# Optimization experiments

Hardware: AMD Instinct MI355X
Metric: run time of the kernel (lower is better)

## Reference

```python
import jax, jax.numpy as jnp
import numpy as np

H = 16  # heads
DH = 64  # dim_head
SCALE = DH ** -0.5


def rotate_half(x):
    x1, x2 = jnp.split(x, 2, axis=-1)
    return jnp.concatenate([-x2, x1], axis=-1)


def apply_rope(pos, t):
    # pos: [n, d] broadcast over [b, h, n, d]
    return t * jnp.cos(pos) + rotate_half(t) * jnp.sin(pos)


def setup_inputs() -> dict:
    key = jax.random.key(0)
    ks = jax.random.split(key, 6)
    B, N, D = 4, 2048, 1024
    inner = H * DH
    x = jax.random.normal(ks[0], (B, N, D), dtype=jnp.float32)
    rotary_emb = jax.random.normal(ks[1], (N, DH), dtype=jnp.float32)
    Wq = jax.random.normal(ks[2], (D, inner), dtype=jnp.float32) / np.sqrt(D)
    Wkv = jax.random.normal(ks[3], (D, 2 * inner), dtype=jnp.float32) / np.sqrt(D)
    Wout = jax.random.normal(ks[4], (inner, D), dtype=jnp.float32) / np.sqrt(inner)
    bout = jnp.zeros((D,), dtype=jnp.float32)
    return {"x": x, "rotary_emb": rotary_emb, "Wq": Wq, "Wkv": Wkv, "Wout": Wout, "bout": bout}


def reference(x, rotary_emb, Wq, Wkv, Wout, bout):
    B, N, D = x.shape
    # QKV projections (self-attention: context = x)
    q = x @ Wq                       # [b, n, h*d]
    kv = x @ Wkv                     # [b, n, 2*h*d]
    k, v = jnp.split(kv, 2, axis=-1)

    def to_heads(t):
        return t.reshape(B, N, H, DH).transpose(0, 2, 1, 3)  # [b, h, n, d]

    q, k, v = to_heads(q), to_heads(k), to_heads(v)
    q = apply_rope(rotary_emb, q)
    k = apply_rope(rotary_emb, k)

    # scaled dot-product attention
    scores = jnp.einsum('bhid,bhjd->bhij', q, k) * SCALE
    attn = jax.nn.softmax(scores, axis=-1)
    out = jnp.einsum('bhij,bhjd->bhid', attn, v)  # [b, h, n, d]
    out = out.transpose(0, 2, 1, 3).reshape(B, N, H * DH)
    return out @ Wout + bout
```

## Files before the change

### kernel.cpp

```cpp
#include <hip/hip_runtime.h>

#define BB 4
#define NN 2048
#define DD 1024
#define HH 16
#define DHH 64
#define MM (BB*NN)
#define QS 3072

typedef unsigned short u16;
typedef __attribute__((ext_vector_type(8))) short short8;
typedef __attribute__((ext_vector_type(4))) float floatx4;

#if __has_builtin(__builtin_amdgcn_exp2f)
#define EXP2F __builtin_amdgcn_exp2f
#else
#define EXP2F exp2f
#endif

__device__ __forceinline__ u16 f2bf(float f) {
  union { float f; unsigned u; } v; v.f = f;
  unsigned u = v.u;
  return (u16)((u + 0x7fffu + ((u >> 16) & 1u)) >> 16);
}
__device__ __forceinline__ float bf2f(u16 h) {
  union { unsigned u; float f; } v; v.u = ((unsigned)h) << 16;
  return v.f;
}
__device__ __forceinline__ unsigned fbits(float f) {
  union { float f; unsigned u; } v; v.f = f; return v.u;
}
__device__ __forceinline__ unsigned pkbf(float lo, float hi) {
#if __has_builtin(__builtin_amdgcn_perm)
  return __builtin_amdgcn_perm(fbits(hi), fbits(lo), 0x07060302u);
#else
  return (fbits(lo) >> 16) | (fbits(hi) & 0xffff0000u);
#endif
}
__device__ __forceinline__ void gll16(const u16* g, u16* l) {
  __builtin_amdgcn_global_load_lds((const __attribute__((address_space(1))) unsigned int*)g,
                                   (__attribute__((address_space(3))) unsigned int*)l, 16, 0, 0);
}
__device__ __forceinline__ int toff(int row, int kc) {
  int pr = row >> 1;
  int c = (((row & 1) << 2) + kc) ^ (pr & 7);
  return pr * 64 + c * 8;
}

#define SOFTMAX_SCALE 0.18033688f
#define SOFTMAX_BIAS  -28.8539008f

__global__ __launch_bounds__(256) void cvt_kernel(const float* __restrict__ in,
                                                  u16* __restrict__ out, int n) {
  int i = (blockIdx.x * 256 + threadIdx.x) * 4;
  if (i >= n) return;
  float4 v = *(const float4*)(in + i);
  u16 o[4] = {f2bf(v.x), f2bf(v.y), f2bf(v.z), f2bf(v.w)};
  *(uint2*)(out + i) = *(uint2*)o;
}

__global__ __launch_bounds__(256) void tcvt3_kernel(const float* __restrict__ Wq,
                                                    const float* __restrict__ Wkv,
                                                    const float* __restrict__ Wout,
                                                    u16* __restrict__ WT,
                                                    u16* __restrict__ WoutT) {
  __shared__ float t[64][65];
  int bx = blockIdx.x;
  const float* src;
  u16* dst;
  int C, c0;
  if (bx < 16)      { src = Wq;   dst = WT;                       C = 1024; c0 = bx * 64; }
  else if (bx < 48) { src = Wkv;  dst = WT + (size_t)DD * DD;     C = 2048; c0 = (bx - 16) * 64; }
  else              { src = Wout; dst = WoutT;                    C = 1024; c0 = (bx - 48) * 64; }
  const int R = 1024;
  int r0 = blockIdx.y * 64;
  int tid = threadIdx.x;
#pragma unroll
  for (int i = 0; i < 16; ++i) {
    int lin = i * 256 + tid;
    int rr = lin >> 6, cc = lin & 63;
    t[rr][cc] = src[(size_t)(r0 + rr) * C + c0 + cc];
  }
  __syncthreads();
#pragma unroll
  for (int i = 0; i < 16; ++i) {
    int lin = i * 256 + tid;
    int rr = lin >> 6, cc = lin & 63;
    dst[(size_t)(c0 + rr) * R + r0 + cc] = f2bf(t[cc][rr]);
  }
}

__global__ __launch_bounds__(256) void rope_tab_kernel(const float* __restrict__ rot,
                                                       float2* __restrict__ tab) {
  int i = blockIdx.x * 256 + threadIdx.x;
  float p = rot[i];
  float s, c;
  __sincosf(p, &s, &c);
  tab[i] = make_float2(c, s);
}

__global__ __launch_bounds__(512, 2) void gemm_qk(const u16* __restrict__ A,
                                                  const u16* __restrict__ Bt,
                                                  u16* __restrict__ qd,
                                                  u16* __restrict__ kd,
                                                  const float2* __restrict__ tab) {
  const int K = DD;
  const int NT = K / 64;
  __shared__ __align__(16) u16 lds[65536];
  int tid = threadIdx.x;
  int wave = tid >> 6, lane = tid & 63;
  int q4 = lane >> 4, l16 = lane & 15;
  int wr = wave >> 2, wc = wave & 3;

  int flat = blockIdx.y * 8 + blockIdx.x;
  int wg = (flat & 7) * 32 + (flat >> 3);
  int bx = wg & 7, by = wg >> 3;
  int m0 = by * 256, n0 = bx * 256;

  const u16* Ag = A + (size_t)m0 * K;
  const u16* Bg = Bt + (size_t)n0 * K;

  int spr = tid >> 3, sct = tid & 7, su = sct ^ (spr & 7);
  int srow = spr * 2 + (su >> 2);
  int skc = (su & 3) * 8;
  size_t so = (size_t)srow * K + skc;

  int toffA[8], toffB[4];
#pragma unroll
  for (int mi = 0; mi < 8; ++mi) toffA[mi] = wr * 4096 + toff(mi * 16 + l16, q4);
#pragma unroll
  for (int ni = 0; ni < 4; ++ni)
    toffB[ni] = (wc >> 1) * 4096 + toff((wc & 1) * 64 + ni * 16 + l16, q4);

  floatx4 acc[8][4];
#pragma unroll
  for (int mi = 0; mi < 8; ++mi)
#pragma unroll
    for (int ni = 0; ni < 4; ++ni) acc[mi][ni] = (floatx4){0.f, 0.f, 0.f, 0.f};

  auto stageHalf = [&](int t, int mat, int kh) {
    const u16* src = (mat ? Bg : Ag) + so + t * 64 + kh * 32;
    u16* dst = lds + (t & 1) * 32768 + mat * 16384 + kh * 8192 + wave * 512;
    gll16(src, dst);
    gll16(src + (size_t)128 * K, dst + 4096);
  };

  stageHalf(0, 1, 0); stageHalf(0, 0, 0); stageHalf(0, 1, 1); stageHalf(0, 0, 1);
  stageHalf(1, 1, 0); stageHalf(1, 0, 0); stageHalf(1, 1, 1);
  __builtin_amdgcn_s_waitcnt(0x0F76);
  __builtin_amdgcn_s_barrier();

#pragma unroll
  for (int t = 0; t < NT; ++t) {
    const u16* Ab = lds + (t & 1) * 32768;
    const u16* Bb = Ab + 16384;
    short8 af[4], bfq[4];

#pragma unroll
    for (int ni = 0; ni < 4; ++ni) bfq[ni] = *(const short8*)(Bb + toffB[ni]);
#pragma unroll
    for (int f = 0; f < 4; ++f) af[f] = *(const short8*)(Ab + toffA[f]);
    if (t + 1 < NT) stageHalf(t + 1, 0, 1);
    __builtin_amdgcn_s_barrier();
    __builtin_amdgcn_s_waitcnt(0xC07F);
    __builtin_amdgcn_s_setprio(1);
#pragma unroll
    for (int f = 0; f < 4; ++f)
#pragma unroll
      for (int ni = 0; ni < 4; ++ni)
        acc[f][ni] = __builtin_amdgcn_mfma_f32_16x16x32_bf16(bfq[ni], af[f], acc[f][ni], 0, 0, 0);
    __builtin_amdgcn_s_setprio(0);
    __builtin_amdgcn_s_barrier();

#pragma unroll
    for (int f = 0; f < 4; ++f) af[f] = *(const short8*)(Ab + toffA[4 + f]);
    if (t + 2 < NT) stageHalf(t + 2, 1, 0);
    __builtin_amdgcn_s_barrier();
    __builtin_amdgcn_s_waitcnt(0xC07F);
    __builtin_amdgcn_s_setprio(1);
#pragma unroll
    for (int f = 0; f < 4; ++f)
#pragma unroll
      for (int ni = 0; ni < 4; ++ni)
        acc[4 + f][ni] = __builtin_amdgcn_mfma_f32_16x16x32_bf16(bfq[ni], af[f], acc[4 + f][ni], 0, 0, 0);
    __builtin_amdgcn_s_setprio(0);
    __builtin_amdgcn_s_barrier();

#pragma unroll
    for (int ni = 0; ni < 4; ++ni) bfq[ni] = *(const short8*)(Bb + 8192 + toffB[ni]);
#pragma unroll
    for (int f = 0; f < 4; ++f) af[f] = *(const short8*)(Ab + 8192 + toffA[f]);
    if (t + 2 < NT) stageHalf(t + 2, 0, 0);
    __builtin_amdgcn_s_barrier();
    __builtin_amdgcn_s_waitcnt(0xC07F);
    __builtin_amdgcn_s_setprio(1);
#pragma unroll
    for (int f = 0; f < 4; ++f)
#pragma unroll
      for (int ni = 0; ni < 4; ++ni)
        acc[f][ni] = __builtin_amdgcn_mfma_f32_16x16x32_bf16(bfq[ni], af[f], acc[f][ni], 0, 0, 0);
    __builtin_amdgcn_s_setprio(0);
    __builtin_amdgcn_s_barrier();

#pragma unroll
    for (int f = 0; f < 4; ++f) af[f] = *(const short8*)(Ab + 8192 + toffA[4 + f]);
    if (t + 2 < NT) stageHalf(t + 2, 1, 1);
    __builtin_amdgcn_s_barrier();
    __builtin_amdgcn_s_waitcnt(0xC07F);
    __builtin_amdgcn_s_setprio(1);
#pragma unroll
    for (int f = 0; f < 4; ++f)
#pragma unroll
      for (int ni = 0; ni < 4; ++ni)
        acc[4 + f][ni] = __builtin_amdgcn_mfma_f32_16x16x32_bf16(bfq[ni], af[f], acc[4 + f][ni], 0, 0, 0);
    __builtin_amdgcn_s_setprio(0);
    if (t == NT - 2) __builtin_amdgcn_s_waitcnt(0x0F70);
    else if (t < NT - 2) __builtin_amdgcn_s_waitcnt(0x0F76);
    __builtin_amdgcn_s_barrier();
  }

  int h = (n0 + wc * 64) >> 6;
  u16* dst = (h < 16) ? qd : kd;
  int hh = h & 15;
  float scl = (h < 16) ? SOFTMAX_SCALE : 1.0f;
  int b = m0 >> 11;
  int tokbase = (m0 & (NN - 1)) + wr * 128;
#pragma unroll
  for (int mi = 0; mi < 8; ++mi) {
    int tok = tokbase + mi * 16 + l16;
    u16* rowp = dst + ((size_t)(b * HH + hh) * NN + tok) * 64;
    const float2* tb = tab + tok * 64;
#pragma unroll
    for (int ni = 0; ni < 2; ++ni) {
      int d0 = ni * 16 + q4 * 4;
      u16 plo[4], phi[4];
#pragma unroll
      for (int r = 0; r < 4; ++r) {
        float2 cs0 = tb[d0 + r];
        float2 cs1 = tb[d0 + r + 32];
        float v0 = acc[mi][ni][r], v1 = acc[mi][ni + 2][r];
        plo[r] = f2bf((v0 * cs0.x - v1 * cs0.y) * scl);
        phi[r] = f2bf((v1 * cs1.x + v0 * cs1.y) * scl);
      }
      *(uint2*)(rowp + d0) = *(uint2*)plo;
      *(uint2*)(rowp + d0 + 32) = *(uint2*)phi;
    }
  }
}

__global__ __launch_bounds__(256) void gemm_v(const u16* __restrict__ A,
                                              const u16* __restrict__ Bt,
                                              u16* __restrict__ vt) {
  const int K = DD;
  __shared__ __align__(16) u16 lds[16384];
  int tid = threadIdx.x;
  int wave = tid >> 6, lane = tid & 63;
  int q4 = lane >> 4, l16 = lane & 15;

  int flat = blockIdx.y * 8 + blockIdx.x;
  int wg = (flat & 7) * 64 + (flat >> 3);
  int bx = wg & 7, by = wg >> 3;
  int m0 = by * 128, n0 = bx * 128;

  int wm = (wave >> 1) * 64, wn = (wave & 1) * 64;

  const u16* Ag = A + (size_t)m0 * K;
  const u16* Bg = Bt + (size_t)(2048 + n0) * K;
  int o1 = tid, o2 = tid + 256;
  int pr1 = o1 >> 3, c1 = (o1 & 7) ^ (pr1 & 7);
  int row1 = pr1 * 2 + (c1 >> 2), kc1 = (c1 & 3) * 8;
  int pr2 = o2 >> 3, c2 = (o2 & 7) ^ (pr2 & 7);
  int row2 = pr2 * 2 + (c2 >> 2), kc2 = (c2 & 3) * 8;
  int d1 = wave * 512, d2 = 2048 + wave * 512;

  int foA[4], foB[4];
#pragma unroll
  for (int i = 0; i < 4; ++i) {
    foA[i] = toff(wm + i * 16 + l16, q4);
    foB[i] = toff(wn + i * 16 + l16, q4);
  }

  floatx4 acc[4][4];
#pragma unroll
  for (int mi = 0; mi < 4; ++mi)
#pragma unroll
    for (int ni = 0; ni < 4; ++ni) acc[mi][ni] = (floatx4){0.f, 0.f, 0.f, 0.f};

  gll16(Ag + (size_t)row1 * K + kc1, lds + d1);
  gll16(Ag + (size_t)row2 * K + kc2, lds + d2);
  gll16(Bg + (size_t)row1 * K + kc1, lds + 8192 + d1);
  gll16(Bg + (size_t)row2 * K + kc2, lds + 8192 + d2);

  for (int k0 = 0, it = 0; k0 < K; k0 += 32, ++it) {
    int boff = (it & 1) * 4096;
    if (k0 + 32 < K) {
      int nboff = 4096 - boff;
      int kn = k0 + 32;
      gll16(Ag + (size_t)row1 * K + kn + kc1, lds + nboff + d1);
      gll16(Ag + (size_t)row2 * K + kn + kc2, lds + nboff + d2);
      gll16(Bg + (size_t)row1 * K + kn + kc1, lds + 8192 + nboff + d1);
      gll16(Bg + (size_t)row2 * K + kn + kc2, lds + 8192 + nboff + d2);
      __builtin_amdgcn_s_waitcnt(0x0F74);
    } else {
      __builtin_amdgcn_s_waitcnt(0x0F70);
    }
    __builtin_amdgcn_s_barrier();
    const u16* Ac = lds + boff;
    const u16* Bc = lds + 8192 + boff;
    short8 af[4], bfr[4];
#pragma unroll
    for (int i = 0; i < 4; ++i) {
      af[i]  = *(const short8*)(Ac + foA[i]);
      bfr[i] = *(const short8*)(Bc + foB[i]);
    }
#pragma unroll
    for (int mi = 0; mi < 4; ++mi)
#pragma unroll
      for (int ni = 0; ni < 4; ++ni)
        acc[mi][ni] = __builtin_amdgcn_mfma_f32_16x16x32_bf16(af[mi], bfr[ni], acc[mi][ni], 0, 0, 0);
    __builtin_amdgcn_s_barrier();
  }

  int h = (n0 + wn) >> 6;
#pragma unroll
  for (int mi = 0; mi < 4; ++mi) {
    int mbase = m0 + wm + mi * 16 + q4 * 4;
    int b = mbase >> 11;
    int nn = mbase & (NN - 1);
    u16* base = vt + (size_t)(b * HH + h) * (NN * 64) + (nn >> 6) * 4096 + (nn & 63);
#pragma unroll
    for (int ni = 0; ni < 4; ++ni) {
      int d = ni * 16 + l16;
      u16 p[4] = {f2bf(acc[mi][ni][0]), f2bf(acc[mi][ni][1]),
                  f2bf(acc[mi][ni][2]), f2bf(acc[mi][ni][3])};
      *(uint2*)(base + d * 64) = *(uint2*)p;
    }
  }
}

__global__ __launch_bounds__(256) void gemm_out(const u16* __restrict__ A,
                                                const u16* __restrict__ Bt,
                                                float* __restrict__ Cout,
                                                const float* __restrict__ bias,
                                                int M, int N, int K) {
  __shared__ __align__(16) u16 lds[16384];
  int tid = threadIdx.x;
  int wave = tid >> 6, lane = tid & 63;
  int q4 = lane >> 4, l16 = lane & 15;
  int m0 = blockIdx.y * 128, n0 = blockIdx.x * 128;
  int wm = (wave >> 1) * 64, wn = (wave & 1) * 64;

  const u16* Ag = A + (size_t)m0 * K;
  const u16* Bg = Bt + (size_t)n0 * K;
  int o1 = tid, o2 = tid + 256;
  int pr1 = o1 >> 3, c1 = (o1 & 7) ^ (pr1 & 7);
  int row1 = pr1 * 2 + (c1 >> 2), kc1 = (c1 & 3) * 8;
  int pr2 = o2 >> 3, c2 = (o2 & 7) ^ (pr2 & 7);
  int row2 = pr2 * 2 + (c2 >> 2), kc2 = (c2 & 3) * 8;
  int d1 = wave * 512, d2 = 2048 + wave * 512;

  int foA[4], foB[4];
#pragma unroll
  for (int i = 0; i < 4; ++i) {
    foA[i] = toff(wm + i * 16 + l16, q4);
    foB[i] = toff(wn + i * 16 + l16, q4);
  }

  floatx4 acc[4][4];
#pragma unroll
  for (int mi = 0; mi < 4; ++mi)
#pragma unroll
    for (int ni = 0; ni < 4; ++ni) acc[mi][ni] = (floatx4){0.f, 0.f, 0.f, 0.f};

  gll16(Ag + (size_t)row1 * K + kc1, lds + d1);
  gll16(Ag + (size_t)row2 * K + kc2, lds + d2);
  gll16(Bg + (size_t)row1 * K + kc1, lds + 8192 + d1);
  gll16(Bg + (size_t)row2 * K + kc2, lds + 8192 + d2);

  for (int k0 = 0, it = 0; k0 < K; k0 += 32, ++it) {
    int boff = (it & 1) * 4096;
    if (k0 + 32 < K) {
      int nboff = 4096 - boff;
      int kn = k0 + 32;
      gll16(Ag + (size_t)row1 * K + kn + kc1, lds + nboff + d1);
      gll16(Ag + (size_t)row2 * K + kn + kc2, lds + nboff + d2);
      gll16(Bg + (size_t)row1 * K + kn + kc1, lds + 8192 + nboff + d1);
      gll16(Bg + (size_t)row2 * K + kn + kc2, lds + 8192 + nboff + d2);
      __builtin_amdgcn_s_waitcnt(0x0F74);
    } else {
      __builtin_amdgcn_s_waitcnt(0x0F70);
    }
    __builtin_amdgcn_s_barrier();
    const u16* Ac = lds + boff;
    const u16* Bc = lds + 8192 + boff;
    short8 af[4], bfr[4];
#pragma unroll
    for (int i = 0; i < 4; ++i) {
      af[i]  = *(const short8*)(Ac + foA[i]);
      bfr[i] = *(const short8*)(Bc + foB[i]);
    }
#pragma unroll
    for (int mi = 0; mi < 4; ++mi)
#pragma unroll
      for (int ni = 0; ni < 4; ++ni)
        acc[mi][ni] = __builtin_amdgcn_mfma_f32_16x16x32_bf16(af[mi], bfr[ni], acc[mi][ni], 0, 0, 0);
    __builtin_amdgcn_s_barrier();
  }

#pragma unroll
  for (int ni = 0; ni < 4; ++ni) {
    int col = n0 + wn + ni * 16 + l16;
    float bval = bias[col];
#pragma unroll
    for (int mi = 0; mi < 4; ++mi) {
#pragma unroll
      for (int r = 0; r < 4; ++r) {
        int row = m0 + wm + mi * 16 + q4 * 4 + r;
        Cout[(size_t)row * N + col] = acc[mi][ni][r] + bval;
      }
    }
  }
}

__global__ __launch_bounds__(512, 4) void attn_kernel(const u16* __restrict__ qd,
                                                      const u16* __restrict__ kd,
                                                      const u16* __restrict__ vt,
                                                      u16* __restrict__ ao) {
  __shared__ __align__(16) u16 lds[16384];

  int tid = threadIdx.x, wave = tid >> 6, lane = tid & 63;
  int q4 = lane >> 4, l16 = lane & 15;
  int qt = blockIdx.x, bh = blockIdx.y, b = bh >> 4, h = bh & 15;
  const u16* qbh = qd + (size_t)bh * NN * 64;
  const u16* kbh = kd + (size_t)bh * NN * 64;
  const u16* vbh = vt + (size_t)bh * NN * 64;

  int srow = wave * 8 + (lane >> 3);
  int g = ((lane & 7) ^ ((lane >> 3) & 7)) * 8;
  int prow = ((srow >> 2) & 3) * 8 + ((srow >> 4) & 1) * 4 + (srow & 3) + ((srow >> 5) & 1) * 32;

#pragma unroll
  for (int it = 0; it < 4; ++it)
    gll16(qbh + (size_t)(qt * 256 + it * 64 + srow) * 64 + g, lds + (it * 64 + wave * 8) * 64);
  __builtin_amdgcn_s_waitcnt(0x0F70);
  __builtin_amdgcn_s_barrier();

  short8 aq[2][2];
#pragma unroll
  for (int mi = 0; mi < 2; ++mi)
#pragma unroll
    for (int ks = 0; ks < 2; ++ks) {
      int row = wave * 32 + mi * 16 + l16;
      aq[mi][ks] = *(const short8*)(lds + row * 64 + (((ks * 4 + q4) ^ (row & 7)) * 8));
    }
  __builtin_amdgcn_s_waitcnt(0xC07F);
  __builtin_amdgcn_s_barrier();

  gll16(kbh + (size_t)prow * 64 + g, lds + wave * 512);
  gll16(vbh + (size_t)srow * 64 + g, lds + 8192 + wave * 512);

  union { unsigned u[4]; short8 s8; } ones;
#pragma unroll
  for (int i = 0; i < 4; ++i) ones.u[i] = 0x3F803F80u;

  floatx4 lacc[2];
  floatx4 o[2][4];
#pragma unroll
  for (int mi = 0; mi < 2; ++mi) {
    lacc[mi] = (floatx4){0.f, 0.f, 0.f, 0.f};
#pragma unroll
    for (int di = 0; di < 4; ++di) o[mi][di] = (floatx4){0.f, 0.f, 0.f, 0.f};
  }

  for (int j0 = 0, itn = 0; j0 < NN; j0 += 64, ++itn) {
    int coff = (itn & 1) * 4096;
    if (j0 + 64 < NN) {
      int noff = 4096 - coff;
      gll16(kbh + (size_t)(j0 + 64 + prow) * 64 + g, lds + noff + wave * 512);
      gll16(vbh + (size_t)((j0 >> 6) + 1) * 4096 + srow * 64 + g, lds + 8192 + noff + wave * 512);
      __builtin_amdgcn_s_waitcnt(0x0F72);
    } else {
      __builtin_amdgcn_s_waitcnt(0x0F70);
    }
    __builtin_amdgcn_s_barrier();

    const u16* Kc = lds + coff;
    const u16* Vc = lds + 8192 + coff;

    floatx4 s[4][2];
#pragma unroll
    for (int kg = 0; kg < 4; ++kg)
#pragma unroll
      for (int mi = 0; mi < 2; ++mi)
        s[kg][mi] = (floatx4){SOFTMAX_BIAS, SOFTMAX_BIAS, SOFTMAX_BIAS, SOFTMAX_BIAS};
#pragma unroll
    for (int ks = 0; ks < 2; ++ks) {
      short8 kf[4];
#pragma unroll
      for (int kg = 0; kg < 4; ++kg) {
        int row = kg * 16 + l16;
        kf[kg] = *(const short8*)(Kc + row * 64 + (((ks * 4 + q4) ^ (row & 7)) * 8));
      }
#pragma unroll
      for (int kg = 0; kg < 4; ++kg)
#pragma unroll
        for (int mi = 0; mi < 2; ++mi)
          s[kg][mi] = __builtin_amdgcn_mfma_f32_16x16x32_bf16(kf[kg], aq[mi][ks], s[kg][mi], 0, 0, 0);
    }

    unsigned pk[4][2][2];
#pragma unroll
    for (int kg = 0; kg < 4; ++kg)
#pragma unroll
      for (int mi = 0; mi < 2; ++mi) {
        float e0 = EXP2F(s[kg][mi][0]);
        float e1 = EXP2F(s[kg][mi][1]);
        float e2 = EXP2F(s[kg][mi][2]);
        float e3 = EXP2F(s[kg][mi][3]);
        pk[kg][mi][0] = pkbf(e0, e1);
        pk[kg][mi][1] = pkbf(e2, e3);
      }

#pragma unroll
    for (int ks = 0; ks < 2; ++ks) {
      short8 vf[4];
#pragma unroll
      for (int di = 0; di < 4; ++di) {
        int row = di * 16 + l16;
        vf[di] = *(const short8*)(Vc + row * 64 + (((ks * 4 + q4) ^ (row & 7)) * 8));
      }
#pragma unroll
      for (int mi = 0; mi < 2; ++mi) {
        union { unsigned u[4]; short8 s8; } bw;
        bw.u[0] = pk[2 * ks][mi][0];
        bw.u[1] = pk[2 * ks][mi][1];
        bw.u[2] = pk[2 * ks + 1][mi][0];
        bw.u[3] = pk[2 * ks + 1][mi][1];
        lacc[mi] = __builtin_amdgcn_mfma_f32_16x16x32_bf16(ones.s8, bw.s8, lacc[mi], 0, 0, 0);
#pragma unroll
        for (int di = 0; di < 4; ++di)
          o[mi][di] = __builtin_amdgcn_mfma_f32_16x16x32_bf16(vf[di], bw.s8, o[mi][di], 0, 0, 0);
      }
    }
    __builtin_amdgcn_s_barrier();
  }

  float rinv[2];
#pragma unroll
  for (int mi = 0; mi < 2; ++mi) rinv[mi] = 1.0f / lacc[mi][0];

#pragma unroll
  for (int mi = 0; mi < 2; ++mi) {
    int qrow = qt * 256 + wave * 32 + mi * 16 + l16;
    size_t base = (size_t)(b * NN + qrow) * DD + h * DHH + q4 * 4;
#pragma unroll
    for (int di = 0; di < 4; ++di)
#pragma unroll
      for (int r = 0; r < 4; ++r)
        ao[base + di * 16 + r] = f2bf(o[mi][di][r] * rinv[mi]);
  }
}

extern "C" void kernel_launch(void* const* d_in, const int* in_sizes, int n_in,
                              void* d_out, int out_size, void* d_ws, size_t ws_size,
                              hipStream_t stream) {
  const float* x    = (const float*)d_in[0];
  const float* rot  = (const float*)d_in[1];
  const float* Wq   = (const float*)d_in[2];
  const float* Wkv  = (const float*)d_in[3];
  const float* Wout = (const float*)d_in[4];
  const float* bout = (const float*)d_in[5];
  float* out = (float*)d_out;

  char* ws = (char*)d_ws;
  size_t off = 0;
  auto alloc = [&](size_t bytes) {
    void* p = ws + off;
    off = (off + bytes + 255) & ~(size_t)255;
    return p;
  };
  u16*    xb    = (u16*)alloc((size_t)MM * DD * 2);
  u16*    WT    = (u16*)alloc((size_t)QS * DD * 2);
  u16*    WoutT = (u16*)alloc((size_t)DD * DD * 2);
  float2* tab   = (float2*)alloc((size_t)NN * DHH * 8);
  u16*    qdb   = (u16*)alloc((size_t)MM * DD * 2);
  u16*    kdb   = (u16*)alloc((size_t)MM * DD * 2);
  u16*    vtt   = (u16*)alloc((size_t)MM * DD * 2);
  u16*    ao    = (u16*)alloc((size_t)MM * DD * 2);

  cvt_kernel<<<(MM * DD / 4) / 256, 256, 0, stream>>>(x, xb, MM * DD);
  tcvt3_kernel<<<dim3(64, 16), 256, 0, stream>>>(Wq, Wkv, Wout, WT, WoutT);
  rope_tab_kernel<<<(NN * DHH) / 256, 256, 0, stream>>>(rot, tab);

  gemm_qk<<<dim3(8, 32), 512, 0, stream>>>(xb, WT, qdb, kdb, tab);
  gemm_v<<<dim3(8, 64), 256, 0, stream>>>(xb, WT, vtt);

  attn_kernel<<<dim3(NN / 256, BB * HH), 512, 0, stream>>>(qdb, kdb, vtt, ao);

  gemm_out<<<dim3(DD / 128, MM / 128), 256, 0, stream>>>(ao, WoutT, out, bout, MM, DD, DD);
}
```

Baseline: 270.6 us.

## Software-pipeline attention loop with 4-stage KV ring and XCD-aware block remap

Restructures the attention main loop so that the QK^T MFMAs for tile t are issued alongside the exp and PV MFMAs for tile t-1, using two score register sets. KV staging grows from double to a 4-slot LDS ring with two tiles of lookahead, and the per-iteration trailing barrier is removed. Blocks are remapped so each XCD handles contiguous heads for L2 reuse, and output stores are vectorized to 8-byte writes. This doubles LDS use to 64KB and raises register pressure, which may lower occupancy below the launch-bounds target.

```diff
diff --git a/kernel.cpp b/kernel.cpp
--- a/kernel.cpp
+++ b/kernel.cpp
@@ -426,11 +426,17 @@
                                                       const u16* __restrict__ kd,
                                                       const u16* __restrict__ vt,
                                                       u16* __restrict__ ao) {
-  __shared__ __align__(16) u16 lds[16384];
+  __shared__ __align__(16) u16 lds[32768];
 
   int tid = threadIdx.x, wave = tid >> 6, lane = tid & 63;
   int q4 = lane >> 4, l16 = lane & 15;
-  int qt = blockIdx.x, bh = blockIdx.y, b = bh >> 4, h = bh & 15;
+
+  int F = blockIdx.y * 8 + blockIdx.x;
+  int xcd = F & 7, r = F >> 3;
+  int bh = xcd * 8 + (r >> 3);
+  int qt = r & 7;
+  int b = bh >> 4, h = bh & 15;
+
   const u16* qbh = qd + (size_t)bh * NN * 64;
   const u16* kbh = kd + (size_t)bh * NN * 64;
   const u16* vbh = vt + (size_t)bh * NN * 64;
@@ -456,8 +462,11 @@
   __builtin_amdgcn_s_waitcnt(0xC07F);
   __builtin_amdgcn_s_barrier();
 
-  gll16(kbh + (size_t)prow * 64 + g, lds + wave * 512);
-  gll16(vbh + (size_t)srow * 64 + g, lds + 8192 + wave * 512);
+  auto stageKV = [&](int t) {
+    gll16(kbh + (size_t)(t * 64 + prow) * 64 + g, lds + (t & 3) * 4096 + wave * 512);
+    gll16(vbh + (size_t)t * 4096 + srow * 64 + g, lds + 16384 + (t & 3) * 4096 + wave * 512);
+  };
+  stageKV(0); stageKV(1);
 
   union { unsigned u[4]; short8 s8; } ones;
 #pragma unroll
@@ -472,22 +481,10 @@
     for (int di = 0; di < 4; ++di) o[mi][di] = (floatx4){0.f, 0.f, 0.f, 0.f};
   }
 
-  for (int j0 = 0, itn = 0; j0 < NN; j0 += 64, ++itn) {
-    int coff = (itn & 1) * 4096;
-    if (j0 + 64 < NN) {
-      int noff = 4096 - coff;
-      gll16(kbh + (size_t)(j0 + 64 + prow) * 64 + g, lds + noff + wave * 512);
-      gll16(vbh + (size_t)((j0 >> 6) + 1) * 4096 + srow * 64 + g, lds + 8192 + noff + wave * 512);
-      __builtin_amdgcn_s_waitcnt(0x0F72);
-    } else {
-      __builtin_amdgcn_s_waitcnt(0x0F70);
-    }
-    __builtin_amdgcn_s_barrier();
-
-    const u16* Kc = lds + coff;
-    const u16* Vc = lds + 8192 + coff;
-
-    floatx4 s[4][2];
+  floatx4 sA[4][2], sB[4][2];
+
+  auto QK = [&](int t, floatx4 (&s)[4][2]) {
+    const u16* Kc = lds + (t & 3) * 4096;
 #pragma unroll
     for (int kg = 0; kg < 4; ++kg)
 #pragma unroll
@@ -507,7 +504,10 @@
         for (int mi = 0; mi < 2; ++mi)
           s[kg][mi] = __builtin_amdgcn_mfma_f32_16x16x32_bf16(kf[kg], aq[mi][ks], s[kg][mi], 0, 0, 0);
     }
-
+  };
+
+  auto EXPPV = [&](int t, floatx4 (&s)[4][2]) {
+    const u16* Vc = lds + 16384 + (t & 3) * 4096;
     unsigned pk[4][2][2];
 #pragma unroll
     for (int kg = 0; kg < 4; ++kg)
@@ -520,7 +520,6 @@
         pk[kg][mi][0] = pkbf(e0, e1);
         pk[kg][mi][1] = pkbf(e2, e3);
       }
-
 #pragma unroll
     for (int ks = 0; ks < 2; ++ks) {
       short8 vf[4];
@@ -542,8 +541,31 @@
           o[mi][di] = __builtin_amdgcn_mfma_f32_16x16x32_bf16(vf[di], bw.s8, o[mi][di], 0, 0, 0);
       }
     }
-    __builtin_amdgcn_s_barrier();
-  }
+  };
+
+  const int NT = NN / 64;
+
+  __builtin_amdgcn_s_waitcnt(0x0F72);
+  __builtin_amdgcn_s_barrier();
+  stageKV(2);
+  QK(0, sA);
+
+  auto iter = [&](int t, floatx4 (&cur)[4][2], floatx4 (&prev)[4][2]) {
+    if (t < NT - 1) __builtin_amdgcn_s_waitcnt(0x0F72);
+    else            __builtin_amdgcn_s_waitcnt(0x0F70);
+    __builtin_amdgcn_s_barrier();
+    if (t + 2 < NT) stageKV(t + 2);
+    QK(t, cur);
+    EXPPV(t - 1, prev);
+  };
+
+  for (int j = 0; j < (NT - 2) / 2; ++j) {
+    int t = 1 + 2 * j;
+    iter(t, sB, sA);
+    iter(t + 1, sA, sB);
+  }
+  iter(NT - 1, sB, sA);
+  EXPPV(NT - 1, sB);
 
   float rinv[2];
 #pragma unroll
@@ -554,10 +576,11 @@
     int qrow = qt * 256 + wave * 32 + mi * 16 + l16;
     size_t base = (size_t)(b * NN + qrow) * DD + h * DHH + q4 * 4;
 #pragma unroll
-    for (int di = 0; di < 4; ++di)
-#pragma unroll
-      for (int r = 0; r < 4; ++r)
-        ao[base + di * 16 + r] = f2bf(o[mi][di][r] * rinv[mi]);
+    for (int di = 0; di < 4; ++di) {
+      u16 p[4] = {f2bf(o[mi][di][0] * rinv[mi]), f2bf(o[mi][di][1] * rinv[mi]),
+                  f2bf(o[mi][di][2] * rinv[mi]), f2bf(o[mi][di][3] * rinv[mi])};
+      *(uint2*)(ao + base + di * 16) = *(uint2*)p;
+    }
   }
 }
 
```

New measurement: 475.4 us. +75.7%, slower.
